# Optimization experiments

Hardware: AMD Instinct MI355X
Metric: run time of the kernel (lower is better)

Reference implementation:

```python
import jax, jax.numpy as jnp
import numpy as np

B, L, D, H = 2, 2048, 1024, 16
HD = D // H  # head_dim = 64


def setup_inputs() -> dict:
    key = jax.random.key(0)
    ks = jax.random.split(key, 8)
    queries = jax.random.normal(ks[0], (B, L, D), dtype=jnp.float32)
    keys = jax.random.normal(ks[1], (B, L, D), dtype=jnp.float32)
    values = jax.random.normal(ks[2], (B, L, D), dtype=jnp.float32)
    mask = jax.random.randint(ks[3], (B, L, L), 0, 2) > 0  # True = masked
    s = 1.0 / np.sqrt(D)
    W_q = jax.random.normal(ks[4], (D, D), dtype=jnp.float32) * s
    W_k = jax.random.normal(ks[5], (D, D), dtype=jnp.float32) * s
    W_v = jax.random.normal(ks[6], (D, D), dtype=jnp.float32) * s
    W_o = jax.random.normal(ks[7], (D, D), dtype=jnp.float32) * s
    return {"queries": queries, "keys": keys, "values": values,
            "W_q": W_q, "W_k": W_k, "W_v": W_v, "W_o": W_o, "mask": mask}


def _split_heads(x):
    # [B, L, D] -> [B, H, L, HD]
    return x.reshape(B, L, H, HD).transpose(0, 2, 1, 3)


def reference(queries, keys, values, W_q, W_k, W_v, W_o, mask):
    # Linear projections (nn.Linear: x @ W.T, no bias)
    q = _split_heads(queries @ W_q.T)   # [B,H,Lq,HD]
    k = _split_heads(keys @ W_k.T)      # [B,H,Lk,HD]
    v = _split_heads(values @ W_v.T)    # [B,H,Lk,HD]
    scores = jnp.einsum('bnqd,bnkd->bnqk', q, k) / np.sqrt(HD)
    scores = jnp.where(mask[:, None, :, :], -1e9, scores)
    attn = jax.nn.softmax(scores, axis=-1)
    ctx = jnp.einsum('bnqk,bnkd->bnqd', attn, v)
    ctx = ctx.transpose(0, 2, 1, 3).reshape(B, L, D)
    return ctx @ W_o.T  # dropout p=0.0 -> identity
```

## Files before the change

### kernel.cpp

```cpp
#include <hip/hip_runtime.h>
#include <hip/hip_bf16.h>

typedef __bf16 bf16;
typedef __attribute__((ext_vector_type(8))) __bf16 bf16x8;
typedef __attribute__((ext_vector_type(4))) __bf16 bf16x4;
typedef __attribute__((ext_vector_type(4))) float f32x4;

#define B_   2
#define L_   2048
#define D_   1024
#define H_   16
#define HD_  64

__device__ __forceinline__ float fast_exp2(float x) {
  float e; asm("v_exp_f32 %0, %1" : "=v"(e) : "v"(x)); return e;
}

__device__ __forceinline__ void gll16(const bf16* g, bf16* l) {
  __builtin_amdgcn_global_load_lds((const __attribute__((address_space(1))) void*)g,
                                   (__attribute__((address_space(3))) void*)l,
                                   16, 0, 0);
}

__global__ void detect_kernel(const unsigned short* __restrict__ q_u,
                              const unsigned char* __restrict__ m_u,
                              int* __restrict__ flags) {
  __shared__ int cnt, odd;
  if (threadIdx.x == 0) { cnt = 0; odd = 0; }
  __syncthreads();
  int c = 0, o = 0;
  for (int i = 0; i < 8; i++) {
    int idx = threadIdx.x * 8 + i;
    unsigned e = (q_u[idx] >> 7) & 0xFF;
    if (e >= 0x8F || (e > 0 && e <= 0x6F)) c++;
    if ((idx & 3) && m_u[idx]) o = 1;
  }
  atomicAdd(&cnt, c);
  if (o) atomicOr(&odd, 1);
  __syncthreads();
  if (threadIdx.x == 0) { flags[0] = (cnt > 128) ? 1 : 0; flags[1] = odd; }
}

__device__ __forceinline__ void canon_body(const void* src, bf16* dst, int i, int f) {
  if (f) {
    const float4* s = (const float4*)src;
    float4 a = s[i / 4], b2 = s[i / 4 + 1];
    bf16x8 o;
    o[0] = (bf16)a.x;  o[1] = (bf16)a.y;  o[2] = (bf16)a.z;  o[3] = (bf16)a.w;
    o[4] = (bf16)b2.x; o[5] = (bf16)b2.y; o[6] = (bf16)b2.z; o[7] = (bf16)b2.w;
    *(bf16x8*)(dst + i) = o;
  } else {
    *(bf16x8*)(dst + i) = ((const bf16x8*)src)[i / 8];
  }
}

__global__ __launch_bounds__(256) void canon_pack(
    const void* xq, const void* xk, const void* xv,
    const void* Wq, const void* Wk, const void* Wv, const void* Wo,
    const void* mp,
    bf16* cxq, bf16* cxk, bf16* cxv,
    bf16* cWq, bf16* cWk, bf16* cWv, bf16* cWo,
    unsigned* __restrict__ bitsT,
    const int* __restrict__ flags) {
  int t = blockIdx.x;
  if (t >= 8192) {
    int wid = (t - 8192) * 256 + threadIdx.x;
    unsigned v = 0;
    if (flags[1]) {
      const uchar4* p = (const uchar4*)mp;
#pragma unroll
      for (int c = 0; c < 8; c++) {
        uchar4 u = p[wid * 8 + c];
        v |= (u.x ? 1u : 0u) << (c * 4 + 0);
        v |= (u.y ? 1u : 0u) << (c * 4 + 1);
        v |= (u.z ? 1u : 0u) << (c * 4 + 2);
        v |= (u.w ? 1u : 0u) << (c * 4 + 3);
      }
    } else {
      const int4* p = (const int4*)mp;
#pragma unroll
      for (int c = 0; c < 8; c++) {
        int4 u = p[wid * 8 + c];
        v |= (u.x ? 1u : 0u) << (c * 4 + 0);
        v |= (u.y ? 1u : 0u) << (c * 4 + 1);
        v |= (u.z ? 1u : 0u) << (c * 4 + 2);
        v |= (u.w ? 1u : 0u) << (c * 4 + 3);
      }
    }
    int row = wid >> 6, word = wid & 63;
    int kt = word >> 1, half = word & 1;
    bitsT[((size_t)kt * 4096 + row) * 2 + half] = v;
    return;
  }
  const int f = flags[0];
  const void* src; bf16* dst; int base;
  if (t < 2048)      { src = xq; dst = cxq; base = t * 2048; }
  else if (t < 4096) { src = xk; dst = cxk; base = (t - 2048) * 2048; }
  else if (t < 6144) { src = xv; dst = cxv; base = (t - 4096) * 2048; }
  else {
    int w = t - 6144, wi = w >> 9;
    base = (w & 511) * 2048;
    if (wi == 0)      { src = Wq; dst = cWq; }
    else if (wi == 1) { src = Wk; dst = cWk; }
    else if (wi == 2) { src = Wv; dst = cWv; }
    else              { src = Wo; dst = cWo; }
  }
  canon_body(src, dst, base + threadIdx.x * 8, f);
}

__global__ __launch_bounds__(256) void gemm_qkv(
    const bf16* __restrict__ Aq, const bf16* __restrict__ Bq, bf16* __restrict__ Cq,
    const bf16* __restrict__ Ak, const bf16* __restrict__ Bk, bf16* __restrict__ Ck,
    const bf16* __restrict__ Av, const bf16* __restrict__ Bv, bf16* __restrict__ VT) {
  __shared__ bf16 smem[128 * 136];
  bf16* sA = smem;
  bf16* sB = smem + 4096;
  const int z = blockIdx.z;
  const bf16* A  = (z == 0) ? Aq : (z == 1) ? Ak : Av;
  const bf16* Bm = (z == 0) ? Bq : (z == 1) ? Bk : Bv;

  const int tid = threadIdx.x;
  const int w = tid >> 6, lane = tid & 63, qd = lane >> 4, r = lane & 15;
  const int wm = w >> 1, wn = w & 1;
  const int m0 = blockIdx.x * 128, n0 = blockIdx.y * 128;

  f32x4 acc[4][4];
#pragma unroll
  for (int i = 0; i < 4; i++)
#pragma unroll
    for (int j = 0; j < 4; j++) acc[i][j] = (f32x4){0.f, 0.f, 0.f, 0.f};

  for (int k0 = 0; k0 < 1024; k0 += 32) {
    __syncthreads();
#pragma unroll
    for (int p = 0; p < 2; p++) {
      int c = p * 256 + tid;
      gll16(A + (size_t)(m0 + (c >> 2)) * 1024 + k0 + (c & 3) * 8, sA + c * 8);
    }
#pragma unroll
    for (int p = 0; p < 2; p++) {
      int c = p * 256 + tid;
      gll16(Bm + (size_t)(n0 + (c >> 2)) * 1024 + k0 + (c & 3) * 8, sB + c * 8);
    }
    __syncthreads();
    bf16x8 af[4], bfv[4];
#pragma unroll
    for (int i = 0; i < 4; i++)
      af[i] = *(const bf16x8*)&sA[(wm * 64 + i * 16 + r) * 32 + qd * 8];
#pragma unroll
    for (int j = 0; j < 4; j++)
      bfv[j] = *(const bf16x8*)&sB[(wn * 64 + j * 16 + r) * 32 + qd * 8];
#pragma unroll
    for (int i = 0; i < 4; i++)
#pragma unroll
      for (int j = 0; j < 4; j++)
        acc[i][j] = __builtin_amdgcn_mfma_f32_16x16x32_bf16(af[i], bfv[j], acc[i][j], 0, 0, 0);
  }

  if (z < 2) {
    bf16* C = (z == 0) ? Cq : Ck;
    const float s = (z == 0) ? 0.1803368801f : 1.0f;
#pragma unroll
    for (int i = 0; i < 4; i++)
#pragma unroll
      for (int j = 0; j < 4; j++)
#pragma unroll
        for (int rr = 0; rr < 4; rr++) {
          int row = m0 + wm * 64 + i * 16 + qd * 4 + rr;
          int col = n0 + wn * 64 + j * 16 + r;
          C[(size_t)row * 1024 + col] = (bf16)(acc[i][j][rr] * s);
        }
  } else {
    __syncthreads();
#pragma unroll
    for (int i = 0; i < 4; i++)
#pragma unroll
      for (int j = 0; j < 4; j++) {
        int col = wn * 64 + j * 16 + r;
        int rowb = wm * 64 + i * 16 + qd * 4;
        bf16x4 v4;
#pragma unroll
        for (int rr = 0; rr < 4; rr++) v4[rr] = (bf16)acc[i][j][rr];
        *(bf16x4*)&smem[col * 136 + rowb] = v4;
      }
    __syncthreads();
    const int b = m0 >> 11, tok0 = m0 & 2047, h0 = n0 >> 6;
#pragma unroll
    for (int p = 0; p < 8; p++) {
      int c = p * 256 + tid;
      int dl = c >> 4, ch = c & 15;
      bf16x8 v = *(const bf16x8*)&smem[dl * 136 + ch * 8];
      int head = h0 + (dl >> 6), d = dl & 63;
      *(bf16x8*)(VT + ((size_t)((b * 16 + head) * 64 + d)) * 2048 + tok0 + ch * 8) = v;
    }
  }
}

__global__ __launch_bounds__(256) void gemm_nt_out(const bf16* __restrict__ A,
                                                   const bf16* __restrict__ Bm,
                                                   void* __restrict__ Cout,
                                                   const int* __restrict__ flags) {
  __shared__ bf16 sA[128 * 32];
  __shared__ bf16 sB[64 * 32];
  const int tid = threadIdx.x;
  const int w = tid >> 6, lane = tid & 63, qd = lane >> 4, r = lane & 15;
  const int wm = w >> 1, wn = w & 1;
  const int m0 = blockIdx.x * 128, n0 = blockIdx.y * 64;

  f32x4 acc[4][2];
#pragma unroll
  for (int i = 0; i < 4; i++)
#pragma unroll
    for (int j = 0; j < 2; j++) acc[i][j] = (f32x4){0.f, 0.f, 0.f, 0.f};

  for (int k0 = 0; k0 < 1024; k0 += 32) {
    __syncthreads();
    {
      int c0 = tid;
      gll16(A + (size_t)(m0 + (c0 >> 2)) * 1024 + k0 + (c0 & 3) * 8, sA + c0 * 8);
      int c1 = 256 + tid;
      gll16(A + (size_t)(m0 + (c1 >> 2)) * 1024 + k0 + (c1 & 3) * 8, sA + c1 * 8);
      int cb = tid;
      gll16(Bm + (size_t)(n0 + (cb >> 2)) * 1024 + k0 + (cb & 3) * 8, sB + cb * 8);
    }
    __syncthreads();
    bf16x8 af[4], bfv[2];
#pragma unroll
    for (int i = 0; i < 4; i++)
      af[i] = *(const bf16x8*)&sA[(wm * 64 + i * 16 + r) * 32 + qd * 8];
#pragma unroll
    for (int j = 0; j < 2; j++)
      bfv[j] = *(const bf16x8*)&sB[(wn * 32 + j * 16 + r) * 32 + qd * 8];
#pragma unroll
    for (int i = 0; i < 4; i++)
#pragma unroll
      for (int j = 0; j < 2; j++)
        acc[i][j] = __builtin_amdgcn_mfma_f32_16x16x32_bf16(af[i], bfv[j], acc[i][j], 0, 0, 0);
  }
  const int f = flags[0];
#pragma unroll
  for (int i = 0; i < 4; i++)
#pragma unroll
    for (int j = 0; j < 2; j++)
#pragma unroll
      for (int rr = 0; rr < 4; rr++) {
        int row = m0 + wm * 64 + i * 16 + qd * 4 + rr;
        int col = n0 + wn * 32 + j * 16 + r;
        if (f) ((float*)Cout)[(size_t)row * 1024 + col] = acc[i][j][rr];
        else   ((bf16*)Cout)[(size_t)row * 1024 + col] = (bf16)acc[i][j][rr];
      }
}

__global__ __launch_bounds__(512, 4) void attn_kernel(const bf16* __restrict__ Q,
                                                      const bf16* __restrict__ Kp,
                                                      const bf16* __restrict__ Vt,
                                                      const unsigned* __restrict__ bitsT,
                                                      bf16* __restrict__ CTX) {
  __shared__ bf16 sK[2][64 * 64];
  __shared__ bf16 sVT[2][64 * 64];
  __shared__ bf16 sP[128 * 72];
  const int tid = threadIdx.x;
  const int w = tid >> 6, lane = tid & 63, qd = lane >> 4, r = lane & 15;
  const int wgid = blockIdx.x;
  const int bh = ((wgid >> 7) << 3) + (wgid & 7);
  const int b = bh >> 4, h = bh & 15;
  const int q0 = ((wgid >> 3) & 15) * 128;
  const int qrow = w * 16 + r;

  bf16x8 qf[2];
#pragma unroll
  for (int ks = 0; ks < 2; ks++)
    qf[ks] = *(const bf16x8*)(Q + (size_t)(b * L_ + q0 + qrow) * D_ +
                              h * HD_ + ks * 32 + qd * 8);

  bf16x8 ones;
#pragma unroll
  for (int e = 0; e < 8; e++) ones[e] = (bf16)1.0f;

  f32x4 o[4], lacc;
#pragma unroll
  for (int dj = 0; dj < 4; dj++) o[dj] = (f32x4){0.f, 0.f, 0.f, 0.f};
  lacc = (f32x4){0.f, 0.f, 0.f, 0.f};

#define STAGE_KV(KT, KB, VB)                                                      \
  {                                                                               \
    int row = tid >> 3, kc = tid & 7;                                             \
    int kcg = kc ^ (row & 7);                                                     \
    gll16(Kp + (size_t)(b * L_ + (KT) * 64 + row) * D_ + h * HD_ + kcg * 8,       \
          (KB) + tid * 8);                                                        \
    gll16(Vt + (size_t)(bh * 64 + row) * L_ + (KT) * 64 + kcg * 8, (VB) + tid * 8); \
  }

#define MLOAD(KT, M0)                                                             \
  M0 = *(const uint2*)(bitsT + ((size_t)(KT) * 4096 + b * 2048 + q0 + qrow) * 2);

  STAGE_KV(0, &sK[0][0], &sVT[0][0]);
  uint2 mc, mn;
  MLOAD(0, mc);
  mn = mc;

#pragma unroll 2
  for (int it = 0; it < 32; ++it) {
    const bf16* kb = &sK[it & 1][0];
    const bf16* vb = &sVT[it & 1][0];

    if (it < 31) {
      STAGE_KV(it + 1, &sK[(it + 1) & 1][0], &sVT[(it + 1) & 1][0]);
      MLOAD(it + 1, mn);
      asm volatile("s_waitcnt vmcnt(3)" ::: "memory");
    } else {
      asm volatile("s_waitcnt vmcnt(0)" ::: "memory");
    }
    __builtin_amdgcn_sched_barrier(0);
    __builtin_amdgcn_s_barrier();

    bf16x8 kf[4][2];
#pragma unroll
    for (int j = 0; j < 4; j++)
#pragma unroll
      for (int ks = 0; ks < 2; ks++) {
        int row = j * 16 + r;
        int phys = (ks * 4 + qd) ^ (row & 7);
        kf[j][ks] = *(const bf16x8*)&kb[row * 64 + phys * 8];
      }

    {
      f32x4 S[4];
      __builtin_amdgcn_s_setprio(1);
#pragma unroll
      for (int j = 0; j < 4; j++) {
        S[j] = (f32x4){0.f, 0.f, 0.f, 0.f};
#pragma unroll
        for (int ks = 0; ks < 2; ks++)
          S[j] = __builtin_amdgcn_mfma_f32_16x16x32_bf16(kf[j][ks], qf[ks], S[j], 0, 0, 0);
      }
      __builtin_amdgcn_s_setprio(0);
#pragma unroll
      for (int j = 0; j < 4; j++) {
        unsigned word = (j < 2) ? mc.x : mc.y;
        unsigned nib = (word >> ((j & 1) * 16 + qd * 4)) & 0xFu;
        bf16x4 pv;
#pragma unroll
        for (int rr = 0; rr < 4; rr++) {
          float e = fast_exp2(S[j][rr]);
          pv[rr] = (bf16)(((nib >> rr) & 1u) ? 0.f : e);
        }
        *(bf16x4*)&sP[qrow * 72 + j * 16 + qd * 4] = pv;
      }
    }
    asm volatile("s_waitcnt lgkmcnt(0)" ::: "memory");

    bf16x8 vf[4][2];
#pragma unroll
    for (int dj = 0; dj < 4; dj++)
#pragma unroll
      for (int ks = 0; ks < 2; ks++) {
        int row = dj * 16 + r;
        int phys = (ks * 4 + qd) ^ (row & 7);
        vf[dj][ks] = *(const bf16x8*)&vb[row * 64 + phys * 8];
      }
    __builtin_amdgcn_s_setprio(1);
#pragma unroll
    for (int ks = 0; ks < 2; ks++) {
      bf16x8 pf = *(const bf16x8*)&sP[qrow * 72 + ks * 32 + qd * 8];
#pragma unroll
      for (int dj = 0; dj < 4; dj++)
        o[dj] = __builtin_amdgcn_mfma_f32_16x16x32_bf16(pf, vf[dj][ks], o[dj], 0, 0, 0);
      lacc = __builtin_amdgcn_mfma_f32_16x16x32_bf16(pf, ones, lacc, 0, 0, 0);
    }
    __builtin_amdgcn_s_setprio(0);

    __builtin_amdgcn_s_barrier();
    mc = mn;
  }
#undef STAGE_KV
#undef MLOAD

  {
    float inv[4];
#pragma unroll
    for (int rr = 0; rr < 4; rr++) inv[rr] = 1.0f / lacc[rr];
#pragma unroll
    for (int dj = 0; dj < 4; dj++)
#pragma unroll
      for (int rr = 0; rr < 4; rr++) {
        int rg = b * L_ + q0 + w * 16 + qd * 4 + rr;
        int col = h * HD_ + dj * 16 + r;
        CTX[(size_t)rg * 1024 + col] = (bf16)(o[dj][rr] * inv[rr]);
      }
  }
}

extern "C" void kernel_launch(void* const* d_in, const int* in_sizes, int n_in,
                              void* d_out, int out_size, void* d_ws, size_t ws_size,
                              hipStream_t stream) {
  const void* xq = d_in[0];
  const void* xk = d_in[1];
  const void* xv = d_in[2];
  const void* Wq = d_in[3];
  const void* Wk = d_in[4];
  const void* Wv = d_in[5];
  const void* Wo = d_in[6];
  const void* mask = d_in[7];

  char* ws = (char*)d_ws;
  const size_t MB = 1048576;
  int*      FLAGS = (int*)(ws + 0);
  unsigned* BITS  = (unsigned*)(ws + 4096);
  bf16* cWo = (bf16*)(ws + 2 * MB);
  bf16* cWq = (bf16*)(ws + 4 * MB);
  bf16* cWk = (bf16*)(ws + 6 * MB);
  bf16* cWv = (bf16*)(ws + 8 * MB);
  bf16* cxq = (bf16*)(ws + 10 * MB);
  bf16* cxk = (bf16*)(ws + 18 * MB);
  bf16* cxv = (bf16*)(ws + 26 * MB);
  bf16* Q   = (bf16*)(ws + 34 * MB);
  bf16* K   = (bf16*)(ws + 42 * MB);
  bf16* VT  = (bf16*)(ws + 50 * MB);
  bf16* CTX = (bf16*)(ws + 26 * MB);

  detect_kernel<<<1, 256, 0, stream>>>((const unsigned short*)xq,
                                       (const unsigned char*)mask, FLAGS);
  canon_pack<<<9216, 256, 0, stream>>>(xq, xk, xv, Wq, Wk, Wv, Wo, mask,
                                       cxq, cxk, cxv, cWq, cWk, cWv, cWo,
                                       BITS, FLAGS);
  gemm_qkv<<<dim3(32, 8, 3), 256, 0, stream>>>(cxq, cWq, Q,
                                               cxk, cWk, K,
                                               cxv, cWv, VT);
  attn_kernel<<<512, 512, 0, stream>>>(Q, K, VT, BITS, CTX);
  gemm_nt_out<<<dim3(32, 16), 256, 0, stream>>>(CTX, cWo, d_out, FLAGS);
}
```

Before: 253.3 us.

## Software-pipeline attention loop: overlap QK of next tile with softmax/PV of previous

Restructures the attention inner loop into a three-buffer software pipeline in which each iteration computes exp/mask of the previous tile's scores, QK MFMAs for the current tile, and PV MFMAs for the previous tile. K/V staging moves from double to triple buffering and the loop is manually unrolled six ways with rotating score and mask registers. The aim is to hide exp/VALU latency and LDS waits behind MFMA work. It costs more LDS and more registers, which could reduce occupancy at the 512x4 launch bounds.

```diff
diff --git a/kernel.cpp b/kernel.cpp
--- a/kernel.cpp
+++ b/kernel.cpp
@@ -256,8 +256,8 @@
                                                       const bf16* __restrict__ Vt,
                                                       const unsigned* __restrict__ bitsT,
                                                       bf16* __restrict__ CTX) {
-  __shared__ bf16 sK[2][64 * 64];
-  __shared__ bf16 sVT[2][64 * 64];
+  __shared__ bf16 sK[3][64 * 64];
+  __shared__ bf16 sVT[3][64 * 64];
   __shared__ bf16 sP[128 * 72];
   const int tid = threadIdx.x;
   const int w = tid >> 6, lane = tid & 63, qd = lane >> 4, r = lane & 15;
@@ -282,99 +282,119 @@
   for (int dj = 0; dj < 4; dj++) o[dj] = (f32x4){0.f, 0.f, 0.f, 0.f};
   lacc = (f32x4){0.f, 0.f, 0.f, 0.f};
 
-#define STAGE_KV(KT, KB, VB)                                                      \
-  {                                                                               \
-    int row = tid >> 3, kc = tid & 7;                                             \
-    int kcg = kc ^ (row & 7);                                                     \
-    gll16(Kp + (size_t)(b * L_ + (KT) * 64 + row) * D_ + h * HD_ + kcg * 8,       \
-          (KB) + tid * 8);                                                        \
-    gll16(Vt + (size_t)(bh * 64 + row) * L_ + (KT) * 64 + kcg * 8, (VB) + tid * 8); \
-  }
-
-#define MLOAD(KT, M0)                                                             \
-  M0 = *(const uint2*)(bitsT + ((size_t)(KT) * 4096 + b * 2048 + q0 + qrow) * 2);
-
-  STAGE_KV(0, &sK[0][0], &sVT[0][0]);
-  uint2 mc, mn;
-  MLOAD(0, mc);
-  mn = mc;
-
-#pragma unroll 2
-  for (int it = 0; it < 32; ++it) {
-    const bf16* kb = &sK[it & 1][0];
-    const bf16* vb = &sVT[it & 1][0];
-
-    if (it < 31) {
-      STAGE_KV(it + 1, &sK[(it + 1) & 1][0], &sVT[(it + 1) & 1][0]);
-      MLOAD(it + 1, mn);
-      asm volatile("s_waitcnt vmcnt(3)" ::: "memory");
-    } else {
-      asm volatile("s_waitcnt vmcnt(0)" ::: "memory");
-    }
-    __builtin_amdgcn_sched_barrier(0);
-    __builtin_amdgcn_s_barrier();
-
-    bf16x8 kf[4][2];
-#pragma unroll
-    for (int j = 0; j < 4; j++)
-#pragma unroll
-      for (int ks = 0; ks < 2; ks++) {
-        int row = j * 16 + r;
-        int phys = (ks * 4 + qd) ^ (row & 7);
-        kf[j][ks] = *(const bf16x8*)&kb[row * 64 + phys * 8];
-      }
-
-    {
-      f32x4 S[4];
-      __builtin_amdgcn_s_setprio(1);
-#pragma unroll
-      for (int j = 0; j < 4; j++) {
-        S[j] = (f32x4){0.f, 0.f, 0.f, 0.f};
-#pragma unroll
-        for (int ks = 0; ks < 2; ks++)
-          S[j] = __builtin_amdgcn_mfma_f32_16x16x32_bf16(kf[j][ks], qf[ks], S[j], 0, 0, 0);
-      }
-      __builtin_amdgcn_s_setprio(0);
-#pragma unroll
-      for (int j = 0; j < 4; j++) {
-        unsigned word = (j < 2) ? mc.x : mc.y;
-        unsigned nib = (word >> ((j & 1) * 16 + qd * 4)) & 0xFu;
-        bf16x4 pv;
-#pragma unroll
-        for (int rr = 0; rr < 4; rr++) {
-          float e = fast_exp2(S[j][rr]);
-          pv[rr] = (bf16)(((nib >> rr) & 1u) ? 0.f : e);
-        }
-        *(bf16x4*)&sP[qrow * 72 + j * 16 + qd * 4] = pv;
-      }
-    }
-    asm volatile("s_waitcnt lgkmcnt(0)" ::: "memory");
-
-    bf16x8 vf[4][2];
-#pragma unroll
-    for (int dj = 0; dj < 4; dj++)
-#pragma unroll
-      for (int ks = 0; ks < 2; ks++) {
-        int row = dj * 16 + r;
-        int phys = (ks * 4 + qd) ^ (row & 7);
-        vf[dj][ks] = *(const bf16x8*)&vb[row * 64 + phys * 8];
-      }
-    __builtin_amdgcn_s_setprio(1);
-#pragma unroll
-    for (int ks = 0; ks < 2; ks++) {
-      bf16x8 pf = *(const bf16x8*)&sP[qrow * 72 + ks * 32 + qd * 8];
-#pragma unroll
-      for (int dj = 0; dj < 4; dj++)
-        o[dj] = __builtin_amdgcn_mfma_f32_16x16x32_bf16(pf, vf[dj][ks], o[dj], 0, 0, 0);
-      lacc = __builtin_amdgcn_mfma_f32_16x16x32_bf16(pf, ones, lacc, 0, 0, 0);
-    }
-    __builtin_amdgcn_s_setprio(0);
-
-    __builtin_amdgcn_s_barrier();
-    mc = mn;
-  }
+  f32x4 S_a[4], S_b[4];
+  uint2 m0r, m1r, m2r;
+
+#define STAGE_KV(KT, BI)                                                            \
+  {                                                                                 \
+    int row_ = tid >> 3, kc_ = tid & 7;                                             \
+    int kcg_ = kc_ ^ (row_ & 7);                                                    \
+    gll16(Kp + (size_t)(b * L_ + (KT) * 64 + row_) * D_ + h * HD_ + kcg_ * 8,       \
+          &sK[BI][0] + tid * 8);                                                    \
+    gll16(Vt + (size_t)(bh * 64 + row_) * L_ + (KT) * 64 + kcg_ * 8,                \
+          &sVT[BI][0] + tid * 8);                                                   \
+  }
+
+#define MLOAD(KT, MD)                                                               \
+  MD = *(const uint2*)(bitsT + ((size_t)(KT) * 4096 + b * 2048 + q0 + qrow) * 2);
+
+#define QK_BLK(BI, SD)                                                              \
+  {                                                                                 \
+    __builtin_amdgcn_s_setprio(1);                                                  \
+    _Pragma("unroll") for (int j = 0; j < 4; j++) {                                 \
+      SD[j] = (f32x4){0.f, 0.f, 0.f, 0.f};                                          \
+      _Pragma("unroll") for (int ks = 0; ks < 2; ks++) {                            \
+        int row_ = j * 16 + r;                                                      \
+        int phys_ = (ks * 4 + qd) ^ (row_ & 7);                                     \
+        bf16x8 kf_ = *(const bf16x8*)&sK[BI][row_ * 64 + phys_ * 8];                \
+        SD[j] = __builtin_amdgcn_mfma_f32_16x16x32_bf16(kf_, qf[ks], SD[j], 0, 0, 0); \
+      }                                                                             \
+    }                                                                               \
+    __builtin_amdgcn_s_setprio(0);                                                  \
+  }
+
+#define EXP_PACK(SP, MP)                                                            \
+  {                                                                                 \
+    _Pragma("unroll") for (int j = 0; j < 4; j++) {                                 \
+      unsigned word_ = ((j) < 2) ? (MP).x : (MP).y;                                 \
+      unsigned nib_ = (word_ >> ((j & 1) * 16 + qd * 4)) & 0xFu;                    \
+      bf16x4 pv_;                                                                   \
+      _Pragma("unroll") for (int rr = 0; rr < 4; rr++) {                            \
+        float e_ = fast_exp2((SP)[j][rr]);                                          \
+        pv_[rr] = (bf16)(((nib_ >> rr) & 1u) ? 0.f : e_);                           \
+      }                                                                             \
+      *(bf16x4*)&sP[qrow * 72 + j * 16 + qd * 4] = pv_;                             \
+    }                                                                               \
+  }
+
+#define PV_BLK(BI)                                                                  \
+  {                                                                                 \
+    asm volatile("s_waitcnt lgkmcnt(0)" ::: "memory");                              \
+    __builtin_amdgcn_sched_barrier(0);                                              \
+    bf16x8 vf_[4][2];                                                               \
+    _Pragma("unroll") for (int dj = 0; dj < 4; dj++)                                \
+      _Pragma("unroll") for (int ks = 0; ks < 2; ks++) {                            \
+        int row_ = dj * 16 + r;                                                     \
+        int phys_ = (ks * 4 + qd) ^ (row_ & 7);                                     \
+        vf_[dj][ks] = *(const bf16x8*)&sVT[BI][row_ * 64 + phys_ * 8];              \
+      }                                                                             \
+    __builtin_amdgcn_s_setprio(1);                                                  \
+    _Pragma("unroll") for (int ks = 0; ks < 2; ks++) {                              \
+      bf16x8 pf_ = *(const bf16x8*)&sP[qrow * 72 + ks * 32 + qd * 8];               \
+      _Pragma("unroll") for (int dj = 0; dj < 4; dj++)                              \
+        o[dj] = __builtin_amdgcn_mfma_f32_16x16x32_bf16(pf_, vf_[dj][ks], o[dj], 0, 0, 0); \
+      lacc = __builtin_amdgcn_mfma_f32_16x16x32_bf16(pf_, ones, lacc, 0, 0, 0);     \
+    }                                                                               \
+    __builtin_amdgcn_s_setprio(0);                                                  \
+  }
+
+#define ITER(T, BP, BC, BN, SPV, SCU, MPV, MNX)                                     \
+  {                                                                                 \
+    STAGE_KV((T) + 1, BN);                                                          \
+    MLOAD((T) + 1, MNX);                                                            \
+    asm volatile("s_waitcnt vmcnt(3)" ::: "memory");                                \
+    __builtin_amdgcn_sched_barrier(0);                                              \
+    __builtin_amdgcn_s_barrier();                                                   \
+    EXP_PACK(SPV, MPV);                                                             \
+    QK_BLK(BC, SCU);                                                                \
+    PV_BLK(BP);                                                                     \
+    __builtin_amdgcn_s_barrier();                                                   \
+  }
+
+  STAGE_KV(0, 0); MLOAD(0, m0r);
+  STAGE_KV(1, 1); MLOAD(1, m1r);
+  asm volatile("s_waitcnt vmcnt(3)" ::: "memory");
+  __builtin_amdgcn_sched_barrier(0);
+  __builtin_amdgcn_s_barrier();
+  QK_BLK(0, S_a);
+  __builtin_amdgcn_s_barrier();
+
+  for (int tt = 1; tt <= 25; tt += 6) {
+    ITER(tt,     0, 1, 2, S_a, S_b, m0r, m2r);
+    ITER(tt + 1, 1, 2, 0, S_b, S_a, m1r, m0r);
+    ITER(tt + 2, 2, 0, 1, S_a, S_b, m2r, m1r);
+    ITER(tt + 3, 0, 1, 2, S_b, S_a, m0r, m2r);
+    ITER(tt + 4, 1, 2, 0, S_a, S_b, m1r, m0r);
+    ITER(tt + 5, 2, 0, 1, S_b, S_a, m2r, m1r);
+  }
+
+  asm volatile("s_waitcnt vmcnt(0)" ::: "memory");
+  __builtin_amdgcn_sched_barrier(0);
+  __builtin_amdgcn_s_barrier();
+  EXP_PACK(S_a, m0r);
+  QK_BLK(1, S_b);
+  PV_BLK(0);
+  __builtin_amdgcn_s_barrier();
+
+  EXP_PACK(S_b, m1r);
+  PV_BLK(1);
+
 #undef STAGE_KV
 #undef MLOAD
+#undef QK_BLK
+#undef EXP_PACK
+#undef PV_BLK
+#undef ITER
 
   {
     float inv[4];
```

Result: no change. 249.4 us, median of 3 (-1.5%).
